# Kernel optimization log

Measured on AMD Instinct MI355X. Metric: run time of the kernel, lower is better.

## Reference

```python
import jax, jax.numpy as jnp
import numpy as np
from functools import partial

D_MODEL = 1024
D_HIDDEN = 4096
N_BLOCKS = 4
D_VOCAB = 32000
BATCH = 2
SEQ = 2048
LN_EPS = 1e-5
LRELU_SLOPE = 0.01  # torch nn.LeakyReLU default


def setup_inputs() -> dict:
    key = jax.random.key(0)
    ks = jax.random.split(key, 16)
    d, h, L, v = D_MODEL, D_HIDDEN, N_BLOCKS, D_VOCAB
    scale = d ** 0.5
    inp = {
        "tokens": jax.random.randint(ks[0], (BATCH, SEQ), 0, v, dtype=jnp.int64)
                  if jax.config.jax_enable_x64 else
                  jax.random.randint(ks[0], (BATCH, SEQ), 0, v, dtype=jnp.int32),
        "emb": jax.random.normal(ks[1], (v, d), jnp.float32) * 0.02,
        # per-block stacked params (leading axis = layer) for lax.scan
        "qk": jax.random.normal(ks[2], (L, d, d), jnp.float32) / scale,
        "ov": jax.random.normal(ks[3], (L, d, d), jnp.float32) / scale,
        "w_up": jax.random.normal(ks[4], (L, d, h), jnp.float32) / scale,
        "b_up": jnp.zeros((L, h), jnp.float32),
        "w_hid": jax.random.normal(ks[5], (L, h, h), jnp.float32) / (h ** 0.5),
        "b_hid": jnp.zeros((L, h), jnp.float32),
        "w_down": jax.random.normal(ks[6], (L, h, d), jnp.float32) / (h ** 0.5),
        "b_down": jnp.zeros((L, d), jnp.float32),
        "ln1_g": jnp.ones((L, d), jnp.float32),
        "ln1_b": jnp.zeros((L, d), jnp.float32),
        "ln2_g": jnp.ones((L, d), jnp.float32),
        "ln2_b": jnp.zeros((L, d), jnp.float32),
    }
    return inp


def _layer_norm(x, g, b):
    mu = jnp.mean(x, axis=-1, keepdims=True)
    var = jnp.mean(jnp.square(x - mu), axis=-1, keepdims=True)
    return (x - mu) * jax.lax.rsqrt(var + LN_EPS) * g + b


def _forward(tokens, emb, qk, ov, w_up, b_up, w_hid, b_hid, w_down, b_down,
             ln1_g, ln1_b, ln2_g, ln2_b):
    x = emb[tokens]                                   # [B, S, D]
    seq = tokens.shape[1]
    scale = jnp.asarray(D_MODEL ** 0.5, x.dtype)
    causal = jnp.tril(jnp.ones((seq, seq), bool))     # True = keep

    def block(x, p):
        (qk, ov, w_up, b_up, w_hid, b_hid, w_down, b_down,
         g1, b1, g2, b2) = p
        h = _layer_norm(x, g1, b1)
        # attention: (h @ qk @ h^T) / sqrt(d), causal mask, softmax, @ h @ ov
        scores = jnp.einsum('bsd,de,bte->bst', h, qk, h) / scale
        scores = jnp.where(causal, scores, -jnp.inf)
        attn = jax.nn.softmax(scores, axis=-1)
        x = x + jnp.einsum('bst,btd,de->bse', attn, h, ov)
        # MLP with LeakyReLU after every layer (incl. output)
        m = _layer_norm(x, g2, b2)
        m = jax.nn.leaky_relu(m @ w_up + b_up, LRELU_SLOPE)
        m = jax.nn.leaky_relu(m @ w_hid + b_hid, LRELU_SLOPE)
        m = jax.nn.leaky_relu(m @ w_down + b_down, LRELU_SLOPE)
        return x + m, None

    params = (qk, ov, w_up, b_up, w_hid, b_hid, w_down, b_down,
              ln1_g, ln1_b, ln2_g, ln2_b)
    x, _ = jax.lax.scan(block, x, params)
    return x @ emb.T                                  # [B, S, V] logits


@jax.jit
def reference(tokens, emb, qk, ov, w_up, b_up, w_hid, b_hid, w_down, b_down,
              ln1_g, ln1_b, ln2_g, ln2_b):
    return _forward(tokens, emb, qk, ov, w_up, b_up, w_hid, b_hid,
                    w_down, b_down, ln1_g, ln1_b, ln2_g, ln2_b)
```

## Files before the change

### kernel.cpp

```cpp
#include <hip/hip_runtime.h>

#define BS   4096
#define SEQL 2048
#define DM   1024
#define DH   4096
#define NV   32000

using u16 = unsigned short;

typedef __attribute__((ext_vector_type(8))) short bf16x8;
typedef __attribute__((ext_vector_type(4))) float f32x4;

__device__ __forceinline__ u16 f2b(float f) {
  union { float f; unsigned u; } c; c.f = f;
  unsigned u = c.u;
  u = (u + 0x7FFFu + ((u >> 16) & 1u)) >> 16;
  return (u16)u;
}

__device__ __forceinline__ void gld16(const u16* g, u16* l) {
  __builtin_amdgcn_global_load_lds(
      (__attribute__((address_space(1))) void*)(void*)const_cast<u16*>(g),
      (__attribute__((address_space(3))) void*)l, 16, 0, 0);
}

__global__ __launch_bounds__(256) void k_embed(const int* __restrict__ tok,
                                               const float* __restrict__ emb,
                                               float* __restrict__ x) {
  const long row = blockIdx.x;
  const long e = tok[row];
  ((float4*)(x + row * DM))[threadIdx.x] = ((const float4*)(emb + e * DM))[threadIdx.x];
}

__global__ __launch_bounds__(256) void k_cvt(const float* __restrict__ in,
                                             u16* __restrict__ out, int n4) {
  int i = blockIdx.x * 256 + threadIdx.x;
  if (i < n4) {
    float4 v = ((const float4*)in)[i];
    ushort4 o;
    o.x = f2b(v.x); o.y = f2b(v.y); o.z = f2b(v.z); o.w = f2b(v.w);
    ((ushort4*)out)[i] = o;
  }
}

__global__ __launch_bounds__(256) void k_ln(const float* __restrict__ x,
                                            const float* __restrict__ g,
                                            const float* __restrict__ b,
                                            u16* __restrict__ out) {
  const long row = blockIdx.x;
  const int t = threadIdx.x;
  float4 v = ((const float4*)(x + row * DM))[t];
  float s  = v.x + v.y + v.z + v.w;
  float q2 = v.x*v.x + v.y*v.y + v.z*v.z + v.w*v.w;
#pragma unroll
  for (int o = 1; o < 64; o <<= 1) { s += __shfl_xor(s, o); q2 += __shfl_xor(q2, o); }
  __shared__ float rs_[4], rq_[4];
  const int lane = t & 63, wid = t >> 6;
  if (lane == 0) { rs_[wid] = s; rq_[wid] = q2; }
  __syncthreads();
  s  = rs_[0] + rs_[1] + rs_[2] + rs_[3];
  q2 = rq_[0] + rq_[1] + rq_[2] + rq_[3];
  const float mu   = s * (1.f / 1024.f);
  const float var  = q2 * (1.f / 1024.f) - mu * mu;
  const float rstd = rsqrtf(var + 1e-5f);
  float4 gg = ((const float4*)g)[t];
  float4 bb = ((const float4*)b)[t];
  ushort4 o;
  o.x = f2b((v.x - mu) * rstd * gg.x + bb.x);
  o.y = f2b((v.y - mu) * rstd * gg.y + bb.y);
  o.z = f2b((v.z - mu) * rstd * gg.z + bb.z);
  o.w = f2b((v.w - mu) * rstd * gg.w + bb.w);
  ((ushort4*)(out + row * DM))[t] = o;
}

__device__ __forceinline__ u16 to_b16(float v) { return f2b(v); }
__device__ __forceinline__ u16 to_b16(u16 v)   { return v; }

template <typename T>
__global__ __launch_bounds__(256) void k_transpose(const T* __restrict__ in,
                                                   u16* __restrict__ out,
                                                   int R, int C, long inz, long outz) {
  __shared__ u16 tile[32][33];
  const T* ip = in + (long)blockIdx.z * inz;
  u16* op = out + (long)blockIdx.z * outz;
  const int tx = threadIdx.x & 31, ty = threadIdx.x >> 5;
  const long c0 = (long)blockIdx.x * 32, r0 = (long)blockIdx.y * 32;
#pragma unroll
  for (int i = 0; i < 4; ++i)
    tile[ty + i * 8][tx] = to_b16(ip[(r0 + ty + i * 8) * C + c0 + tx]);
  __syncthreads();
#pragma unroll
  for (int i = 0; i < 4; ++i)
    op[(c0 + ty + i * 8) * R + r0 + tx] = tile[tx][ty + i * 8];
}

__global__ __launch_bounds__(256) void k_softmax(const float* __restrict__ sc,
                                                 u16* __restrict__ at) {
  const int r = blockIdx.x;
  const long z = blockIdx.y;
  const int t = threadIdx.x;
  const float* row = sc + (z * SEQL + r) * SEQL;
  u16* orow = at + (z * SEQL + r) * SEQL;
  const int ni = (r >> 8) + 1;
  float vals[8];
  float mx = -3.4e38f;
  for (int i = 0; i < ni; ++i) {
    int c = i * 256 + t;
    float v = (c <= r) ? row[c] : -3.4e38f;
    vals[i] = v;
    mx = fmaxf(mx, v);
  }
#pragma unroll
  for (int o = 1; o < 64; o <<= 1) mx = fmaxf(mx, __shfl_xor(mx, o));
  __shared__ float rm[4], rsum[4];
  const int lane = t & 63, wid = t >> 6;
  if (lane == 0) rm[wid] = mx;
  __syncthreads();
  mx = fmaxf(fmaxf(rm[0], rm[1]), fmaxf(rm[2], rm[3]));
  float sum = 0.f;
  for (int i = 0; i < ni; ++i) {
    int c = i * 256 + t;
    float e = (c <= r) ? __expf(vals[i] - mx) : 0.f;
    vals[i] = e;
    sum += e;
  }
#pragma unroll
  for (int o = 1; o < 64; o <<= 1) sum += __shfl_xor(sum, o);
  if (lane == 0) rsum[wid] = sum;
  __syncthreads();
  sum = rsum[0] + rsum[1] + rsum[2] + rsum[3];
  const float inv = 1.f / sum;
  for (int i = 0; i < ni; ++i) orow[i * 256 + t] = f2b(vals[i] * inv);
}

template <int EPI, bool BIAS, bool LRELU, int CAUSAL>
__global__ __launch_bounds__(256, 2) void k_gemm_bt(
    const u16* __restrict__ A, const u16* __restrict__ B, void* __restrict__ C,
    const float* __restrict__ bias, int K, int N,
    long sAz, long sBz, long sCz, float scale) {
  __shared__ u16 lA[128 * 32];
  __shared__ u16 lB[128 * 32];
  const int t = threadIdx.x;
  const long z = blockIdx.z;
  const long row0 = (long)blockIdx.x * 128;
  const long col0 = (long)blockIdx.y * 128;
  if (CAUSAL == 1 && col0 > row0 + 127) return;
  const int Klim = (CAUSAL == 2) ? min(K, (int)row0 + 128) : K;
  const u16* Ab = A + z * sAz;
  const u16* Bb = B + z * sBz;

  const int rr = t >> 2;
  const int c8 = (t & 3) * 8;
  const u16* gA0 = Ab + (row0 + rr) * K + c8;
  const u16* gA1 = Ab + (row0 + 64 + rr) * K + c8;
  const u16* gB0 = Bb + (col0 + rr) * K + c8;
  const u16* gB1 = Bb + (col0 + 64 + rr) * K + c8;
  u16* sA0 = &lA[rr * 32 + c8];
  u16* sA1 = &lA[(64 + rr) * 32 + c8];
  u16* sB0 = &lB[rr * 32 + c8];
  u16* sB1 = &lB[(64 + rr) * 32 + c8];

  const int lane = t & 63;
  const int w = t >> 6;
  const int wr = (w >> 1) * 64, wc = (w & 1) * 64;
  const int fr = lane & 15;
  const int fk = (lane >> 4) * 8;

  f32x4 acc[4][4] = {};

  for (int k0 = 0; k0 < Klim; k0 += 32) {
    gld16(gA0 + k0, sA0);
    gld16(gA1 + k0, sA1);
    gld16(gB0 + k0, sB0);
    gld16(gB1 + k0, sB1);
    __syncthreads();
    bf16x8 av[4], bv[4];
#pragma unroll
    for (int m = 0; m < 4; ++m) av[m] = *(const bf16x8*)&lA[(wr + m * 16 + fr) * 32 + fk];
#pragma unroll
    for (int n = 0; n < 4; ++n) bv[n] = *(const bf16x8*)&lB[(wc + n * 16 + fr) * 32 + fk];
#pragma unroll
    for (int m = 0; m < 4; ++m)
#pragma unroll
      for (int n = 0; n < 4; ++n)
        acc[m][n] = __builtin_amdgcn_mfma_f32_16x16x32_bf16(av[m], bv[n], acc[m][n], 0, 0, 0);
    __syncthreads();
  }

  const int er = (lane >> 4) * 4;
  const int ec = lane & 15;
#pragma unroll
  for (int m = 0; m < 4; ++m) {
#pragma unroll
    for (int n = 0; n < 4; ++n) {
#pragma unroll
      for (int j = 0; j < 4; ++j) {
        long r = row0 + wr + m * 16 + er + j;
        long c = col0 + wc + n * 16 + ec;
        float v = acc[m][n][j] * scale;
        if (BIAS)  v += bias[c];
        if (LRELU) v = v > 0.f ? v : 0.01f * v;
        if (EPI == 0)      ((float*)C)[z * sCz + r * (long)N + c] = v;
        else if (EPI == 1) ((u16*)C)[z * sCz + r * (long)N + c] = f2b(v);
        else               ((float*)C)[z * sCz + r * (long)N + c] += v;
      }
    }
  }
}

template <int EPI, bool BIAS, bool LRELU>
__global__ __launch_bounds__(512, 1) void k_gemm256(
    const u16* __restrict__ A, const u16* __restrict__ B, void* __restrict__ C,
    const float* __restrict__ bias, int K, int N, float scale) {
  __shared__ u16 S[65536];
  char* Sc = (char*)&S[0];
  const int t = threadIdx.x;
  const int lane = t & 63;
  const int w = t >> 6;
  const int wr = w >> 2;
  const int wc = w & 3;
  const long row0 = (long)blockIdx.x * 256;
  const long col0 = (long)blockIdx.y * 256;
  const int nt = K >> 6;

  int srow[2], scol[2], ldsb[2];
#pragma unroll
  for (int i = 0; i < 2; ++i) {
    int d = t * 16 + i * 8192;
    int dx = d ^ (((d >> 7) & 3) << 4);
    srow[i] = dx >> 6;
    scol[i] = (dx & 63) >> 1;
    ldsb[i] = d;
  }
  const u16* Abase = A + row0 * (long)K;
  const u16* Bbase = B + col0 * (long)K;

  auto stage = [&](int opb, int kh, int buf, int kb) {
#pragma unroll
    for (int i = 0; i < 2; ++i) {
      const u16* src = (opb ? Bbase : Abase) + (long)srow[i] * K + kb + kh * 32 + scol[i];
      u16* dst = &S[(buf * 4 + opb * 2 + kh) * 8192 + (ldsb[i] >> 1)];
      gld16(src, dst);
    }
  };

  const int fr = lane & 15;
  const int fky = lane >> 4;
  const int axor = ((fr >> 1) & 3) << 4;
  int aoff[8], boff[4];
#pragma unroll
  for (int m = 0; m < 8; ++m)
    aoff[m] = (((wr * 128 + m * 16 + fr) * 64) + fky * 16) ^ axor;
#pragma unroll
  for (int n = 0; n < 4; ++n)
    boff[n] = (((wc * 64 + n * 16 + fr) * 64) + fky * 16) ^ axor;

  f32x4 acc[8][4] = {};
  bf16x8 aA0, aA1, aA2, aA3, aB0, aB1, aB2, aB3;
  bf16x8 bX0, bX1, bX2, bX3, bY0, bY1, bY2, bY3;

#define RD_A(d0, d1, d2, d3, bb, kh, mh)                                   \
  { const char* Ah_ = Sc + (bb) * 65536 + (kh) * 16384;                    \
    d0 = *(const bf16x8*)(Ah_ + aoff[(mh) * 4 + 0]);                       \
    d1 = *(const bf16x8*)(Ah_ + aoff[(mh) * 4 + 1]);                       \
    d2 = *(const bf16x8*)(Ah_ + aoff[(mh) * 4 + 2]);                       \
    d3 = *(const bf16x8*)(Ah_ + aoff[(mh) * 4 + 3]); }
#define RD_B(d0, d1, d2, d3, bb, kh)                                       \
  { const char* Bh_ = Sc + (bb) * 65536 + 32768 + (kh) * 16384;            \
    d0 = *(const bf16x8*)(Bh_ + boff[0]);                                  \
    d1 = *(const bf16x8*)(Bh_ + boff[1]);                                  \
    d2 = *(const bf16x8*)(Bh_ + boff[2]);                                  \
    d3 = *(const bf16x8*)(Bh_ + boff[3]); }
#define MF16(a0, a1, a2, a3, b0, b1, b2, b3, mh)                                                     \
  __builtin_amdgcn_s_setprio(1);                                                                     \
  acc[(mh)*4+0][0] = __builtin_amdgcn_mfma_f32_16x16x32_bf16(a0, b0, acc[(mh)*4+0][0], 0, 0, 0);     \
  acc[(mh)*4+0][1] = __builtin_amdgcn_mfma_f32_16x16x32_bf16(a0, b1, acc[(mh)*4+0][1], 0, 0, 0);     \
  acc[(mh)*4+0][2] = __builtin_amdgcn_mfma_f32_16x16x32_bf16(a0, b2, acc[(mh)*4+0][2], 0, 0, 0);     \
  acc[(mh)*4+0][3] = __builtin_amdgcn_mfma_f32_16x16x32_bf16(a0, b3, acc[(mh)*4+0][3], 0, 0, 0);     \
  acc[(mh)*4+1][0] = __builtin_amdgcn_mfma_f32_16x16x32_bf16(a1, b0, acc[(mh)*4+1][0], 0, 0, 0);     \
  acc[(mh)*4+1][1] = __builtin_amdgcn_mfma_f32_16x16x32_bf16(a1, b1, acc[(mh)*4+1][1], 0, 0, 0);     \
  acc[(mh)*4+1][2] = __builtin_amdgcn_mfma_f32_16x16x32_bf16(a1, b2, acc[(mh)*4+1][2], 0, 0, 0);     \
  acc[(mh)*4+1][3] = __builtin_amdgcn_mfma_f32_16x16x32_bf16(a1, b3, acc[(mh)*4+1][3], 0, 0, 0);     \
  acc[(mh)*4+2][0] = __builtin_amdgcn_mfma_f32_16x16x32_bf16(a2, b0, acc[(mh)*4+2][0], 0, 0, 0);     \
  acc[(mh)*4+2][1] = __builtin_amdgcn_mfma_f32_16x16x32_bf16(a2, b1, acc[(mh)*4+2][1], 0, 0, 0);     \
  acc[(mh)*4+2][2] = __builtin_amdgcn_mfma_f32_16x16x32_bf16(a2, b2, acc[(mh)*4+2][2], 0, 0, 0);     \
  acc[(mh)*4+2][3] = __builtin_amdgcn_mfma_f32_16x16x32_bf16(a2, b3, acc[(mh)*4+2][3], 0, 0, 0);     \
  acc[(mh)*4+3][0] = __builtin_amdgcn_mfma_f32_16x16x32_bf16(a3, b0, acc[(mh)*4+3][0], 0, 0, 0);     \
  acc[(mh)*4+3][1] = __builtin_amdgcn_mfma_f32_16x16x32_bf16(a3, b1, acc[(mh)*4+3][1], 0, 0, 0);     \
  acc[(mh)*4+3][2] = __builtin_amdgcn_mfma_f32_16x16x32_bf16(a3, b2, acc[(mh)*4+3][2], 0, 0, 0);     \
  acc[(mh)*4+3][3] = __builtin_amdgcn_mfma_f32_16x16x32_bf16(a3, b3, acc[(mh)*4+3][3], 0, 0, 0);     \
  __builtin_amdgcn_s_setprio(0);

  stage(0, 0, 0, 0);
  stage(1, 0, 0, 0);
  stage(0, 1, 0, 0);
  stage(1, 1, 0, 0);
  asm volatile("s_waitcnt vmcnt(4)" ::: "memory");
  __builtin_amdgcn_s_barrier();
  RD_A(aA0, aA1, aA2, aA3, 0, 0, 0);
  RD_B(bX0, bX1, bX2, bX3, 0, 0);

  int cur = 0;
  for (int tt = 0; tt < nt; ++tt) {
    const int knext = (tt + 1 < nt ? tt + 1 : tt) * 64;
    const int nx = cur ^ 1;
    RD_A(aB0, aB1, aB2, aB3, cur, 0, 1);
    stage(0, 0, nx, knext);
    MF16(aA0, aA1, aA2, aA3, bX0, bX1, bX2, bX3, 0);
    asm volatile("s_waitcnt vmcnt(2)" ::: "memory");
    __builtin_amdgcn_s_barrier();
    RD_A(aA0, aA1, aA2, aA3, cur, 1, 0);
    RD_B(bY0, bY1, bY2, bY3, cur, 1);
    stage(1, 0, nx, knext);
    MF16(aB0, aB1, aB2, aB3, bX0, bX1, bX2, bX3, 1);
    __builtin_amdgcn_s_barrier();
    RD_A(aB0, aB1, aB2, aB3, cur, 1, 1);
    stage(0, 1, nx, knext);
    MF16(aA0, aA1, aA2, aA3, bY0, bY1, bY2, bY3, 0);
    asm volatile("s_waitcnt vmcnt(2)" ::: "memory");
    __builtin_amdgcn_s_barrier();
    RD_A(aA0, aA1, aA2, aA3, nx, 0, 0);
    RD_B(bX0, bX1, bX2, bX3, nx, 0);
    stage(1, 1, nx, knext);
    MF16(aB0, aB1, aB2, aB3, bY0, bY1, bY2, bY3, 1);
    __builtin_amdgcn_s_barrier();
    cur = nx;
  }
  asm volatile("s_waitcnt vmcnt(0)" ::: "memory");
#undef RD_A
#undef RD_B
#undef MF16

  const int er = (lane >> 4) * 4;
  const int ec = lane & 15;
#pragma unroll
  for (int m = 0; m < 8; ++m) {
#pragma unroll
    for (int n = 0; n < 4; ++n) {
#pragma unroll
      for (int j = 0; j < 4; ++j) {
        long r = row0 + wr * 128 + m * 16 + er + j;
        long c = col0 + wc * 64 + n * 16 + ec;
        float v = acc[m][n][j] * scale;
        if (BIAS)  v += bias[c];
        if (LRELU) v = v > 0.f ? v : 0.01f * v;
        if (EPI == 0)      ((float*)C)[r * (long)N + c] = v;
        else if (EPI == 1) ((u16*)C)[r * (long)N + c] = f2b(v);
        else               ((float*)C)[r * (long)N + c] += v;
      }
    }
  }
}

extern "C" void kernel_launch(void* const* d_in, const int* in_sizes, int n_in,
                              void* d_out, int out_size, void* d_ws, size_t ws_size,
                              hipStream_t stream) {
  const int*   tokens = (const int*)d_in[0];
  const float* emb    = (const float*)d_in[1];
  const float* qk     = (const float*)d_in[2];
  const float* ov     = (const float*)d_in[3];
  const float* wup    = (const float*)d_in[4];
  const float* bup    = (const float*)d_in[5];
  const float* whid   = (const float*)d_in[6];
  const float* bhid   = (const float*)d_in[7];
  const float* wdown  = (const float*)d_in[8];
  const float* bdown  = (const float*)d_in[9];
  const float* g1     = (const float*)d_in[10];
  const float* b1     = (const float*)d_in[11];
  const float* g2     = (const float*)d_in[12];
  const float* b2     = (const float*)d_in[13];

  char* Ob = (char*)d_out;
  float* scores = (float*)(Ob + 0);
  u16*   attn   = (u16*)(Ob + 33554432);
  u16*   m1     = (u16*)(Ob + 50331648);
  u16*   m2     = (u16*)(Ob + 83886080);
  u16*   qkT    = (u16*)(Ob + 117440512);
  u16*   ovT    = (u16*)(Ob + 125829120);
  u16*   upT    = (u16*)(Ob + 134217728);
  u16*   hidT   = (u16*)(Ob + 167772160);
  u16*   downT  = (u16*)(Ob + 301989888);
  float* xres   = (float*)(Ob + 335544320);
  u16*   h      = (u16*)(Ob + 352321536);
  u16*   hT     = (u16*)(Ob + 360710144);
  u16*   q      = (u16*)(Ob + 369098752);
  u16*   attnV  = (u16*)(Ob + 377487360);

  u16* embB = (u16*)d_ws;
  u16* xB   = (u16*)((char*)d_ws + 65536000);

  k_embed<<<dim3(BS), 256, 0, stream>>>(tokens, emb, xres);
  k_cvt<<<dim3(32000), 256, 0, stream>>>(emb, embB, 8192000);

  k_transpose<float><<<dim3(32, 32, 4),   256, 0, stream>>>(qk,    qkT,   1024, 1024, 1048576,  1048576);
  k_transpose<float><<<dim3(32, 32, 4),   256, 0, stream>>>(ov,    ovT,   1024, 1024, 1048576,  1048576);
  k_transpose<float><<<dim3(128, 32, 4),  256, 0, stream>>>(wup,   upT,   1024, 4096, 4194304,  4194304);
  k_transpose<float><<<dim3(128, 128, 4), 256, 0, stream>>>(whid,  hidT,  4096, 4096, 16777216, 16777216);
  k_transpose<float><<<dim3(32, 128, 4),  256, 0, stream>>>(wdown, downT, 4096, 1024, 4194304,  4194304);

  for (int l = 0; l < 4; ++l) {
    k_ln<<<dim3(BS), 256, 0, stream>>>(xres, g1 + l * 1024, b1 + l * 1024, h);
    k_transpose<u16><<<dim3(32, 64, 2), 256, 0, stream>>>(h, hT, 2048, 1024, 2048L * 1024, 1024L * 2048);
    k_gemm_bt<1, false, false, 0><<<dim3(32, 8, 1), 256, 0, stream>>>(
        h, qkT + (long)l * 1048576, q, nullptr, 1024, 1024, 0, 0, 0, 0.03125f);
    k_gemm_bt<0, false, false, 1><<<dim3(16, 16, 2), 256, 0, stream>>>(
        q, h, scores, nullptr, 1024, 2048, 2048L * 1024, 2048L * 1024, 2048L * 2048, 1.f);
    k_softmax<<<dim3(2048, 2), 256, 0, stream>>>(scores, attn);
    k_gemm_bt<1, false, false, 2><<<dim3(16, 8, 2), 256, 0, stream>>>(
        attn, hT, attnV, nullptr, 2048, 1024, 2048L * 2048, 1024L * 2048, 2048L * 1024, 1.f);
    k_gemm_bt<2, false, false, 0><<<dim3(32, 8, 1), 256, 0, stream>>>(
        attnV, ovT + (long)l * 1048576, xres, nullptr, 1024, 1024, 0, 0, 0, 1.f);

    k_ln<<<dim3(BS), 256, 0, stream>>>(xres, g2 + l * 1024, b2 + l * 1024, h);
    k_gemm256<1, true, true><<<dim3(16, 16), 512, 0, stream>>>(
        h, upT + (long)l * 4194304, m1, bup + l * 4096, 1024, 4096, 1.f);
    k_gemm256<1, true, true><<<dim3(16, 16), 512, 0, stream>>>(
        m1, hidT + (long)l * 16777216, m2, bhid + l * 4096, 4096, 4096, 1.f);
    k_gemm_bt<2, true, true, 0><<<dim3(32, 8, 1), 256, 0, stream>>>(
        m2, downT + (long)l * 4194304, xres, bdown + l * 1024, 4096, 1024, 0, 0, 0, 1.f);
  }

  k_cvt<<<dim3(4096), 256, 0, stream>>>(xres, xB, 1048576);
  k_gemm256<0, false, false><<<dim3(16, 125), 512, 0, stream>>>(
      xB, embB, (float*)d_out, nullptr, 1024, 32000, 1.f);
}
```

Before: 2.181 ms.

## Use 64x64 transpose tiles, fuse final bf16 cast, add extra barriers in hidden GEMM

The transpose kernel now works on 64x64 tiles, so fewer blocks are launched and each thread moves more elements. The last layer's down-projection epilogue writes the bf16 copy of the residual directly, which removes the separate conversion kernel before the logits GEMM. The 256-tile GEMM body is split into separate kernels, and the hidden-layer one gets an extra barrier after each stage issue, which may keep the waves in lockstep but adds synchronisation cost.

New measurement: 2.152 ms. Within noise of the previous version (-1.3%).

```diff
diff --git a/kernel.cpp b/kernel.cpp
--- a/kernel.cpp
+++ b/kernel.cpp
@@ -77,21 +77,21 @@
 __device__ __forceinline__ u16 to_b16(u16 v)   { return v; }
 
 template <typename T>
-__global__ __launch_bounds__(256) void k_transpose(const T* __restrict__ in,
-                                                   u16* __restrict__ out,
-                                                   int R, int C, long inz, long outz) {
-  __shared__ u16 tile[32][33];
+__global__ __launch_bounds__(256) void k_transpose64(const T* __restrict__ in,
+                                                     u16* __restrict__ out,
+                                                     int R, int C, long inz, long outz) {
+  __shared__ u16 tile[64][65];
   const T* ip = in + (long)blockIdx.z * inz;
   u16* op = out + (long)blockIdx.z * outz;
-  const int tx = threadIdx.x & 31, ty = threadIdx.x >> 5;
-  const long c0 = (long)blockIdx.x * 32, r0 = (long)blockIdx.y * 32;
-#pragma unroll
-  for (int i = 0; i < 4; ++i)
-    tile[ty + i * 8][tx] = to_b16(ip[(r0 + ty + i * 8) * C + c0 + tx]);
+  const int tx = threadIdx.x & 63, ty = threadIdx.x >> 6;
+  const long c0 = (long)blockIdx.x * 64, r0 = (long)blockIdx.y * 64;
+#pragma unroll
+  for (int i = 0; i < 16; ++i)
+    tile[ty + i * 4][tx] = to_b16(ip[(r0 + ty + i * 4) * C + c0 + tx]);
   __syncthreads();
 #pragma unroll
-  for (int i = 0; i < 4; ++i)
-    op[(c0 + ty + i * 8) * R + r0 + tx] = tile[tx][ty + i * 8];
+  for (int i = 0; i < 16; ++i)
+    op[(c0 + ty + i * 4) * R + r0 + tx] = tile[tx][ty + i * 4];
 }
 
 __global__ __launch_bounds__(256) void k_softmax(const float* __restrict__ sc,
@@ -133,10 +133,10 @@
   for (int i = 0; i < ni; ++i) orow[i * 256 + t] = f2b(vals[i] * inv);
 }
 
-template <int EPI, bool BIAS, bool LRELU, int CAUSAL>
+template <int EPI, bool BIAS, bool LRELU, int CAUSAL, bool XOUT>
 __global__ __launch_bounds__(256, 2) void k_gemm_bt(
     const u16* __restrict__ A, const u16* __restrict__ B, void* __restrict__ C,
-    const float* __restrict__ bias, int K, int N,
+    const float* __restrict__ bias, u16* __restrict__ xb, int K, int N,
     long sAz, long sBz, long sCz, float scale) {
   __shared__ u16 lA[128 * 32];
   __shared__ u16 lB[128 * 32];
@@ -200,20 +200,24 @@
         float v = acc[m][n][j] * scale;
         if (BIAS)  v += bias[c];
         if (LRELU) v = v > 0.f ? v : 0.01f * v;
-        if (EPI == 0)      ((float*)C)[z * sCz + r * (long)N + c] = v;
-        else if (EPI == 1) ((u16*)C)[z * sCz + r * (long)N + c] = f2b(v);
-        else               ((float*)C)[z * sCz + r * (long)N + c] += v;
+        long idx = z * sCz + r * (long)N + c;
+        if (EPI == 0)      ((float*)C)[idx] = v;
+        else if (EPI == 1) ((u16*)C)[idx] = f2b(v);
+        else {
+          float nv = ((float*)C)[idx] + v;
+          ((float*)C)[idx] = nv;
+          if (XOUT) xb[idx] = f2b(nv);
+        }
       }
     }
   }
 }
 
-template <int EPI, bool BIAS, bool LRELU>
-__global__ __launch_bounds__(512, 1) void k_gemm256(
-    const u16* __restrict__ A, const u16* __restrict__ B, void* __restrict__ C,
-    const float* __restrict__ bias, int K, int N, float scale) {
-  __shared__ u16 S[65536];
-  char* Sc = (char*)&S[0];
+template <int EPI, bool BIAS, bool LRELU, bool BAR2>
+__device__ __forceinline__ void g256_body(
+    u16* S, const u16* __restrict__ A, const u16* __restrict__ B,
+    void* __restrict__ C, const float* __restrict__ bias, int K, int N, float scale) {
+  char* Sc = (char*)S;
   const int t = threadIdx.x;
   const int lane = t & 63;
   const int w = t >> 6;
@@ -306,22 +310,26 @@
     const int nx = cur ^ 1;
     RD_A(aB0, aB1, aB2, aB3, cur, 0, 1);
     stage(0, 0, nx, knext);
+    if (BAR2) __builtin_amdgcn_s_barrier();
     MF16(aA0, aA1, aA2, aA3, bX0, bX1, bX2, bX3, 0);
     asm volatile("s_waitcnt vmcnt(2)" ::: "memory");
     __builtin_amdgcn_s_barrier();
     RD_A(aA0, aA1, aA2, aA3, cur, 1, 0);
     RD_B(bY0, bY1, bY2, bY3, cur, 1);
     stage(1, 0, nx, knext);
+    if (BAR2) __builtin_amdgcn_s_barrier();
     MF16(aB0, aB1, aB2, aB3, bX0, bX1, bX2, bX3, 1);
     __builtin_amdgcn_s_barrier();
     RD_A(aB0, aB1, aB2, aB3, cur, 1, 1);
     stage(0, 1, nx, knext);
+    if (BAR2) __builtin_amdgcn_s_barrier();
     MF16(aA0, aA1, aA2, aA3, bY0, bY1, bY2, bY3, 0);
     asm volatile("s_waitcnt vmcnt(2)" ::: "memory");
     __builtin_amdgcn_s_barrier();
     RD_A(aA0, aA1, aA2, aA3, nx, 0, 0);
     RD_B(bX0, bX1, bX2, bX3, nx, 0);
     stage(1, 1, nx, knext);
+    if (BAR2) __builtin_amdgcn_s_barrier();
     MF16(aB0, aB1, aB2, aB3, bY0, bY1, bY2, bY3, 1);
     __builtin_amdgcn_s_barrier();
     cur = nx;
@@ -350,6 +358,25 @@
       }
     }
   }
+}
+
+__global__ __launch_bounds__(512, 1) void k_g256_up(
+    const u16* __restrict__ A, const u16* __restrict__ B, void* __restrict__ C,
+    const float* __restrict__ bias, int K, int N, float scale) {
+  __shared__ u16 S[65536];
+  g256_body<1, true, true, false>(S, A, B, C, bias, K, N, scale);
+}
+__global__ __launch_bounds__(512, 1) void k_g256_hid(
+    const u16* __restrict__ A, const u16* __restrict__ B, void* __restrict__ C,
+    const float* __restrict__ bias, int K, int N, float scale) {
+  __shared__ u16 S[65536];
+  g256_body<1, true, true, true>(S, A, B, C, bias, K, N, scale);
+}
+__global__ __launch_bounds__(512, 1) void k_g256_log(
+    const u16* __restrict__ A, const u16* __restrict__ B, void* __restrict__ C,
+    const float* __restrict__ bias, int K, int N, float scale) {
+  __shared__ u16 S[65536];
+  g256_body<0, false, false, false>(S, A, B, C, bias, K, N, scale);
 }
 
 extern "C" void kernel_launch(void* const* d_in, const int* in_sizes, int n_in,
@@ -392,35 +419,39 @@
   k_embed<<<dim3(BS), 256, 0, stream>>>(tokens, emb, xres);
   k_cvt<<<dim3(32000), 256, 0, stream>>>(emb, embB, 8192000);
 
-  k_transpose<float><<<dim3(32, 32, 4),   256, 0, stream>>>(qk,    qkT,   1024, 1024, 1048576,  1048576);
-  k_transpose<float><<<dim3(32, 32, 4),   256, 0, stream>>>(ov,    ovT,   1024, 1024, 1048576,  1048576);
-  k_transpose<float><<<dim3(128, 32, 4),  256, 0, stream>>>(wup,   upT,   1024, 4096, 4194304,  4194304);
-  k_transpose<float><<<dim3(128, 128, 4), 256, 0, stream>>>(whid,  hidT,  4096, 4096, 16777216, 16777216);
-  k_transpose<float><<<dim3(32, 128, 4),  256, 0, stream>>>(wdown, downT, 4096, 1024, 4194304,  4194304);
+  k_transpose64<float><<<dim3(16, 16, 4), 256, 0, stream>>>(qk,    qkT,   1024, 1024, 1048576,  1048576);
+  k_transpose64<float><<<dim3(16, 16, 4), 256, 0, stream>>>(ov,    ovT,   1024, 1024, 1048576,  1048576);
+  k_transpose64<float><<<dim3(64, 16, 4), 256, 0, stream>>>(wup,   upT,   1024, 4096, 4194304,  4194304);
+  k_transpose64<float><<<dim3(64, 64, 4), 256, 0, stream>>>(whid,  hidT,  4096, 4096, 16777216, 16777216);
+  k_transpose64<float><<<dim3(16, 64, 4), 256, 0, stream>>>(wdown, downT, 4096, 1024, 4194304,  4194304);
 
   for (int l = 0; l < 4; ++l) {
     k_ln<<<dim3(BS), 256, 0, stream>>>(xres, g1 + l * 1024, b1 + l * 1024, h);
-    k_transpose<u16><<<dim3(32, 64, 2), 256, 0, stream>>>(h, hT, 2048, 1024, 2048L * 1024, 1024L * 2048);
-    k_gemm_bt<1, false, false, 0><<<dim3(32, 8, 1), 256, 0, stream>>>(
-        h, qkT + (long)l * 1048576, q, nullptr, 1024, 1024, 0, 0, 0, 0.03125f);
-    k_gemm_bt<0, false, false, 1><<<dim3(16, 16, 2), 256, 0, stream>>>(
-        q, h, scores, nullptr, 1024, 2048, 2048L * 1024, 2048L * 1024, 2048L * 2048, 1.f);
+    k_transpose64<u16><<<dim3(16, 32, 2), 256, 0, stream>>>(h, hT, 2048, 1024, 2048L * 1024, 1024L * 2048);
+    k_gemm_bt<1, false, false, 0, false><<<dim3(32, 8, 1), 256, 0, stream>>>(
+        h, qkT + (long)l * 1048576, q, nullptr, nullptr, 1024, 1024, 0, 0, 0, 0.03125f);
+    k_gemm_bt<0, false, false, 1, false><<<dim3(16, 16, 2), 256, 0, stream>>>(
+        q, h, scores, nullptr, nullptr, 1024, 2048, 2048L * 1024, 2048L * 1024, 2048L * 2048, 1.f);
     k_softmax<<<dim3(2048, 2), 256, 0, stream>>>(scores, attn);
-    k_gemm_bt<1, false, false, 2><<<dim3(16, 8, 2), 256, 0, stream>>>(
-        attn, hT, attnV, nullptr, 2048, 1024, 2048L * 2048, 1024L * 2048, 2048L * 1024, 1.f);
-    k_gemm_bt<2, false, false, 0><<<dim3(32, 8, 1), 256, 0, stream>>>(
-        attnV, ovT + (long)l * 1048576, xres, nullptr, 1024, 1024, 0, 0, 0, 1.f);
+    k_gemm_bt<1, false, false, 2, false><<<dim3(16, 8, 2), 256, 0, stream>>>(
+        attn, hT, attnV, nullptr, nullptr, 2048, 1024, 2048L * 2048, 1024L * 2048, 2048L * 1024, 1.f);
+    k_gemm_bt<2, false, false, 0, false><<<dim3(32, 8, 1), 256, 0, stream>>>(
+        attnV, ovT + (long)l * 1048576, xres, nullptr, nullptr, 1024, 1024, 0, 0, 0, 1.f);
 
     k_ln<<<dim3(BS), 256, 0, stream>>>(xres, g2 + l * 1024, b2 + l * 1024, h);
-    k_gemm256<1, true, true><<<dim3(16, 16), 512, 0, stream>>>(
+    k_g256_up<<<dim3(16, 16), 512, 0, stream>>>(
         h, upT + (long)l * 4194304, m1, bup + l * 4096, 1024, 4096, 1.f);
-    k_gemm256<1, true, true><<<dim3(16, 16), 512, 0, stream>>>(
+    k_g256_hid<<<dim3(16, 16), 512, 0, stream>>>(
         m1, hidT + (long)l * 16777216, m2, bhid + l * 4096, 4096, 4096, 1.f);
-    k_gemm_bt<2, true, true, 0><<<dim3(32, 8, 1), 256, 0, stream>>>(
-        m2, downT + (long)l * 4194304, xres, bdown + l * 1024, 4096, 1024, 0, 0, 0, 1.f);
-  }
-
-  k_cvt<<<dim3(4096), 256, 0, stream>>>(xres, xB, 1048576);
-  k_gemm256<0, false, false><<<dim3(16, 125), 512, 0, stream>>>(
+    if (l == 3) {
+      k_gemm_bt<2, true, true, 0, true><<<dim3(32, 8, 1), 256, 0, stream>>>(
+          m2, downT + (long)l * 4194304, xres, bdown + l * 1024, xB, 4096, 1024, 0, 0, 0, 1.f);
+    } else {
+      k_gemm_bt<2, true, true, 0, false><<<dim3(32, 8, 1), 256, 0, stream>>>(
+          m2, downT + (long)l * 4194304, xres, bdown + l * 1024, nullptr, 4096, 1024, 0, 0, 0, 1.f);
+    }
+  }
+
+  k_g256_log<<<dim3(16, 125), 512, 0, stream>>>(
       xB, embB, (float*)d_out, nullptr, 1024, 32000, 1.f);
 }
```
